# Kernel optimization log

Measured on AMD Instinct MI355X. Metric: run time of the kernel, lower is better.

Reference implementation:

```python
import jax, jax.numpy as jnp
import numpy as np

EPS = 1e-12  # torch F.normalize eps


def _l2norm(v, axis):
    return v / jnp.maximum(jnp.linalg.norm(v, axis=axis, keepdims=True), EPS)


def setup_inputs() -> dict:
    key = jax.random.key(0)
    k1, k2, k3 = jax.random.split(key, 3)
    N, D, H, W, K = 32, 512, 64, 64, 64
    x = jax.random.normal(k1, (N, D, H, W), dtype=jnp.float32)
    conv_w = jax.random.normal(k2, (K, D), dtype=jnp.float32) * 0.05
    centroids = jax.random.normal(k3, (K, D), dtype=jnp.float32)
    return {"x": x, "conv_w": conv_w, "centroids": centroids}


def reference(x, conv_w, centroids):
    # x: [N, D, H, W]; conv_w: [K, D] (1x1 conv, no bias); centroids: [K, D]
    N, D, H, W = x.shape
    K = conv_w.shape[0]
    # descriptor-wise L2 normalization over channel dim
    x = _l2norm(x, axis=1)
    xf = x.reshape(N, D, H * W)                      # [N, D, P]
    # 1x1 conv == matmul over channels; softmax over clusters
    logits = jnp.einsum('kd,ndp->nkp', conv_w, xf)    # [N, K, P]
    a = jax.nn.softmax(logits, axis=1)                # [N, K, P]
    # vlad[n,k,d] = sum_p a[n,k,p] * (xf[n,d,p] - c[k,d])
    #            = (a @ xf^T)[n,k,d] - (sum_p a[n,k,p]) * c[k,d]
    vlad = jnp.einsum('nkp,ndp->nkd', a, xf) \
         - a.sum(axis=-1)[:, :, None] * centroids[None, :, :]  # [N, K, D]
    vlad = _l2norm(vlad, axis=2)                      # intra-normalization
    v = vlad.reshape(N, K * D)
    return _l2norm(v, axis=1)                         # global L2 norm
```

## Files before the change

### kernel.cpp

```cpp
#include <hip/hip_runtime.h>
#include <hip/hip_bf16.h>
#include <math.h>

#define Nn 32
#define Dd 512
#define Pp 4096
#define Kk 64
#define SEG 16
#define PXB 256
#define PT 64
static constexpr float EPSF = 1e-12f;

typedef short short8 __attribute__((ext_vector_type(8)));
typedef short short4v __attribute__((ext_vector_type(4)));
typedef float floatx4 __attribute__((ext_vector_type(4)));

static __device__ __forceinline__ int f2b2(float a, float b) {
  __hip_bfloat162 h = __float22bfloat162_rn(float2{a, b});
  int r; __builtin_memcpy(&r, &h, 4); return r;
}
static __device__ __forceinline__ short8 pack8(const float* v) {
  union { short8 s; int i[4]; } u;
  u.i[0] = f2b2(v[0], v[1]); u.i[1] = f2b2(v[2], v[3]);
  u.i[2] = f2b2(v[4], v[5]); u.i[3] = f2b2(v[6], v[7]);
  return u.s;
}
static __device__ __forceinline__ short f2b1(float f) {
  unsigned u = __float_as_uint(f);
  return (short)((u + 0x7FFFu + ((u >> 16) & 1u)) >> 16);
}
static __device__ __forceinline__ float b2f(short s) {
  return __uint_as_float(((unsigned)(unsigned short)s) << 16);
}

__global__ __launch_bounds__(256) void k_wpack(
    const float* __restrict__ w, short* __restrict__ wp)
{
  int id = blockIdx.x * 256 + threadIdx.x;
  int chunk = id >> 6, k = id & 63;
  const float* src = w + (size_t)k * Dd + chunk * 32;
  short* dst = wp + ((size_t)(chunk * 64 + k)) * 32;
#pragma unroll
  for (int q = 0; q < 4; ++q) {
    float v[8];
    *(float4*)&v[0] = *(const float4*)(src + q * 8);
    *(float4*)&v[4] = *(const float4*)(src + q * 8 + 4);
    *(short8*)(dst + q * 8) = pack8(v);
  }
}

__global__ __launch_bounds__(256, 2) void k_fused(
    const float* __restrict__ x, const short* __restrict__ wp,
    float* __restrict__ asum, short* __restrict__ vpart)
{
  constexpr int XS = 64;
  constexpr int AS = 72;
  __shared__ short xb[Dd * XS];
  __shared__ short as_[Kk * AS];
  __shared__ float invs[PT];

  const int tid = threadIdx.x;
  const int n = blockIdx.x >> 4, seg = blockIdx.x & 15;
  const int wave = tid >> 6, lane = tid & 63;
  const int q = lane >> 4, pc = lane & 15;
  const int sd = tid >> 3, sc = tid & 7;

  floatx4 acc2[4][8];
#pragma unroll
  for (int t = 0; t < 4; ++t)
#pragma unroll
    for (int s2 = 0; s2 < 8; ++s2) acc2[t][s2] = floatx4{0.f, 0.f, 0.f, 0.f};
  float asr[4] = {0.f, 0.f, 0.f, 0.f};

  const float* xn = x + (size_t)n * Dd * Pp;

  for (int pt = 0; pt < PXB / PT; ++pt) {
    const int p0 = seg * PXB + pt * PT;
    __syncthreads();

    floatx4 acc1[4];
#pragma unroll
    for (int t = 0; t < 4; ++t) acc1[t] = floatx4{0.f, 0.f, 0.f, 0.f};
    float sq = 0.f;

    const float* xa = xn + (size_t)(q * 8) * Pp + p0 + wave * 16 + pc;
    const float* xs = xn + (size_t)sd * Pp + p0 + sc * 8;

    for (int dc = 0; dc < Dd; dc += 32) {
      float4 u0 = *(const float4*)xs;
      float4 u1 = *(const float4*)(xs + 4);
      int2 w0 = { f2b2(u0.x, u0.y), f2b2(u0.z, u0.w) };
      int2 w1 = { f2b2(u1.x, u1.y), f2b2(u1.z, u1.w) };
      *(int2*)&xb[(dc + sd) * XS + sc * 8] = w0;
      *(int2*)&xb[(dc + sd) * XS + sc * 8 + 4] = w1;
      xs += (size_t)32 * Pp;
      float v[8];
#pragma unroll
      for (int j = 0; j < 8; ++j) {
        float a = xa[(size_t)j * Pp];
        v[j] = a; sq += a * a;
      }
      xa += (size_t)32 * Pp;
      short8 af = pack8(v);
      const short* wc = wp + (size_t)(dc >> 5) * 2048 + pc * 32 + q * 8;
#pragma unroll
      for (int t = 0; t < 4; ++t) {
        short8 bf = *(const short8*)(wc + t * 512);
        acc1[t] = __builtin_amdgcn_mfma_f32_16x16x32_bf16(af, bf, acc1[t], 0, 0, 0);
      }
    }

    {
      float tsum = sq;
      tsum += __shfl_xor(tsum, 16);
      tsum += __shfl_xor(tsum, 32);
      if (q == 0) invs[wave * 16 + pc] = 1.f / fmaxf(sqrtf(tsum), EPSF);
    }
    float ivr[4];
#pragma unroll
    for (int r = 0; r < 4; ++r) ivr[r] = invs[wave * 16 + q * 4 + r];

#pragma unroll
    for (int r = 0; r < 4; ++r) {
      float l[4];
#pragma unroll
      for (int t = 0; t < 4; ++t) l[t] = acc1[t][r] * ivr[r];
      float mx = fmaxf(fmaxf(l[0], l[1]), fmaxf(l[2], l[3]));
      mx = fmaxf(mx, __shfl_xor(mx, 1));
      mx = fmaxf(mx, __shfl_xor(mx, 2));
      mx = fmaxf(mx, __shfl_xor(mx, 4));
      mx = fmaxf(mx, __shfl_xor(mx, 8));
      float e[4], sm = 0.f;
#pragma unroll
      for (int t = 0; t < 4; ++t) { e[t] = __expf(l[t] - mx); sm += e[t]; }
      sm += __shfl_xor(sm, 1);
      sm += __shfl_xor(sm, 2);
      sm += __shfl_xor(sm, 4);
      sm += __shfl_xor(sm, 8);
      float si = 1.f / sm;
#pragma unroll
      for (int t = 0; t < 4; ++t) {
        float av = e[t] * si;
        asr[t] += av;
        as_[(t * 16 + pc) * AS + wave * 16 + q * 4 + r] = f2b1(av * ivr[r]);
      }
    }
    __syncthreads();

#pragma unroll
    for (int c = 0; c < 2; ++c) {
      short8 af2[4];
#pragma unroll
      for (int t = 0; t < 4; ++t)
        af2[t] = *(const short8*)&as_[(t * 16 + pc) * AS + c * 32 + q * 8];
#pragma unroll
      for (int s2 = 0; s2 < 8; ++s2) {
        short8 bf2 = *(const short8*)&xb[(wave * 128 + s2 * 16 + pc) * XS + c * 32 + q * 8];
#pragma unroll
        for (int t = 0; t < 4; ++t)
          acc2[t][s2] = __builtin_amdgcn_mfma_f32_16x16x32_bf16(af2[t], bf2, acc2[t][s2], 0, 0, 0);
      }
    }
  }

#pragma unroll
  for (int t = 0; t < 4; ++t) {
    float v = asr[t];
    v += __shfl_xor(v, 16);
    v += __shfl_xor(v, 32);
    if (q == 0) atomicAdd(&asum[n * Kk + t * 16 + pc], v);
  }
  short* vb = vpart + ((size_t)(seg * Nn + n) * Kk) * Dd;
#pragma unroll
  for (int t = 0; t < 4; ++t)
#pragma unroll
    for (int s2 = 0; s2 < 8; ++s2)
#pragma unroll
      for (int r = 0; r < 4; ++r)
        vb[(size_t)(t * 16 + q * 4 + r) * Dd + wave * 128 + s2 * 16 + pc] =
            f2b1(acc2[t][s2][r]);
}

__global__ __launch_bounds__(128) void k_intra(
    const short* __restrict__ vpart, const float* __restrict__ asum,
    const float* __restrict__ cent, float* __restrict__ out, float* __restrict__ gnsq)
{
  __shared__ float red[2];
  const int nk = blockIdx.x;
  const int n = nk >> 6, k = nk & 63;
  const int tid = threadIdx.x;
  const int d = tid * 4;

  float4 v = {0.f, 0.f, 0.f, 0.f};
#pragma unroll
  for (int ps = 0; ps < SEG; ++ps) {
    short4v t = *(const short4v*)&vpart[((size_t)(ps * Nn + n) * Kk + k) * Dd + d];
    v.x += b2f(t[0]); v.y += b2f(t[1]); v.z += b2f(t[2]); v.w += b2f(t[3]);
  }
  float s = asum[n * Kk + k];
  float4 c = *(const float4*)&cent[(size_t)k * Dd + d];
  v.x -= s * c.x; v.y -= s * c.y; v.z -= s * c.z; v.w -= s * c.w;

  float qq = v.x * v.x + v.y * v.y + v.z * v.z + v.w * v.w;
#pragma unroll
  for (int off = 32; off; off >>= 1) qq += __shfl_down(qq, off);
  if ((tid & 63) == 0) red[tid >> 6] = qq;
  __syncthreads();
  float norm = sqrtf(red[0] + red[1]);
  float r = 1.f / fmaxf(norm, EPSF);
  v.x *= r; v.y *= r; v.z *= r; v.w *= r;
  *(float4*)&out[(size_t)n * (Kk * Dd) + (size_t)k * Dd + d] = v;
  if (tid == 0) {
    float t = norm * r;
    atomicAdd(&gnsq[n], t * t);
  }
}

__global__ __launch_bounds__(256) void k_gscale(
    float* __restrict__ out, const float* __restrict__ gnsq)
{
  size_t i = ((size_t)blockIdx.x * 256 + threadIdx.x) * 4;
  int n = (int)(i >> 15);
  float r = 1.f / fmaxf(sqrtf(gnsq[n]), EPSF);
  float4 v = *(float4*)&out[i];
  v.x *= r; v.y *= r; v.z *= r; v.w *= r;
  *(float4*)&out[i] = v;
}

extern "C" void kernel_launch(void* const* d_in, const int* in_sizes, int n_in,
                              void* d_out, int out_size, void* d_ws, size_t ws_size,
                              hipStream_t stream) {
  (void)in_sizes; (void)n_in; (void)out_size; (void)ws_size;
  const float* x    = (const float*)d_in[0];
  const float* w    = (const float*)d_in[1];
  const float* cent = (const float*)d_in[2];
  float* out = (float*)d_out;

  float* asum  = (float*)d_ws;
  float* gnsq  = asum + Nn * Kk;
  short* vpart = (short*)(gnsq + 64);
  short* wpk   = vpart + (size_t)SEG * Nn * Kk * Dd;

  hipMemsetAsync(asum, 0, (Nn * Kk + 64) * sizeof(float), stream);
  k_wpack<<<4, 256, 0, stream>>>(w, wpk);
  k_fused<<<Nn * SEG, 256, 0, stream>>>(x, wpk, asum, vpart);
  k_intra<<<Nn * Kk, 128, 0, stream>>>(vpart, asum, cent, out, gnsq);
  k_gscale<<<(Nn * Kk * Dd) / (256 * 4), 256, 0, stream>>>(out, gnsq);
}
```

Measured before the change: 421.0 us.

## Split k_fused clusters across 8 waves, swizzle LDS, fold global norm into constant

```diff
diff --git a/kernel.cpp b/kernel.cpp
--- a/kernel.cpp
+++ b/kernel.cpp
@@ -34,9 +34,12 @@
 }
 
 __global__ __launch_bounds__(256) void k_wpack(
-    const float* __restrict__ w, short* __restrict__ wp)
+    const float* __restrict__ w, float* __restrict__ asum,
+    short* __restrict__ wp)
 {
   int id = blockIdx.x * 256 + threadIdx.x;
+  if (id >= 1024) return;
+  asum[id] = 0.f; asum[id + 1024] = 0.f;
   int chunk = id >> 6, k = id & 63;
   const float* src = w + (size_t)k * Dd + chunk * 32;
   short* dst = wp + ((size_t)(chunk * 64 + k)) * 32;
@@ -49,7 +52,7 @@
   }
 }
 
-__global__ __launch_bounds__(256, 2) void k_fused(
+__global__ __launch_bounds__(512, 4) void k_fused(
     const float* __restrict__ x, const short* __restrict__ wp,
     float* __restrict__ asum, short* __restrict__ vpart)
 {
@@ -58,19 +61,23 @@
   __shared__ short xb[Dd * XS];
   __shared__ short as_[Kk * AS];
   __shared__ float invs[PT];
+  __shared__ float ssum[2 * PT];
 
   const int tid = threadIdx.x;
   const int n = blockIdx.x >> 4, seg = blockIdx.x & 15;
   const int wave = tid >> 6, lane = tid & 63;
+  const int wg = wave & 3, kh = wave >> 2;
   const int q = lane >> 4, pc = lane & 15;
-  const int sd = tid >> 3, sc = tid & 7;
-
-  floatx4 acc2[4][8];
-#pragma unroll
-  for (int t = 0; t < 4; ++t)
-#pragma unroll
-    for (int s2 = 0; s2 < 8; ++s2) acc2[t][s2] = floatx4{0.f, 0.f, 0.f, 0.f};
-  float asr[4] = {0.f, 0.f, 0.f, 0.f};
+  const int sd = tid >> 4, sc = tid & 15;
+  const int swcol = (sc * 4) ^ ((sd & 7) << 3);
+  const int rdxor = (pc & 7) << 3;
+
+  floatx4 acc2[4][4];
+#pragma unroll
+  for (int a = 0; a < 4; ++a)
+#pragma unroll
+    for (int b = 0; b < 4; ++b) acc2[a][b] = floatx4{0.f, 0.f, 0.f, 0.f};
+  float asr[2] = {0.f, 0.f};
 
   const float* xn = x + (size_t)n * Dd * Pp;
 
@@ -78,21 +85,18 @@
     const int p0 = seg * PXB + pt * PT;
     __syncthreads();
 
-    floatx4 acc1[4];
-#pragma unroll
-    for (int t = 0; t < 4; ++t) acc1[t] = floatx4{0.f, 0.f, 0.f, 0.f};
+    floatx4 acc1[2];
+    acc1[0] = floatx4{0.f, 0.f, 0.f, 0.f};
+    acc1[1] = floatx4{0.f, 0.f, 0.f, 0.f};
     float sq = 0.f;
 
-    const float* xa = xn + (size_t)(q * 8) * Pp + p0 + wave * 16 + pc;
-    const float* xs = xn + (size_t)sd * Pp + p0 + sc * 8;
+    const float* xa = xn + (size_t)(q * 8) * Pp + p0 + wg * 16 + pc;
+    const float* xs = xn + (size_t)sd * Pp + p0 + sc * 4;
 
     for (int dc = 0; dc < Dd; dc += 32) {
       float4 u0 = *(const float4*)xs;
-      float4 u1 = *(const float4*)(xs + 4);
-      int2 w0 = { f2b2(u0.x, u0.y), f2b2(u0.z, u0.w) };
-      int2 w1 = { f2b2(u1.x, u1.y), f2b2(u1.z, u1.w) };
-      *(int2*)&xb[(dc + sd) * XS + sc * 8] = w0;
-      *(int2*)&xb[(dc + sd) * XS + sc * 8 + 4] = w1;
+      *(int2*)&xb[(dc + sd) * XS + swcol] =
+          int2{ f2b2(u0.x, u0.y), f2b2(u0.z, u0.w) };
       xs += (size_t)32 * Pp;
       float v[8];
 #pragma unroll
@@ -102,48 +106,44 @@
       }
       xa += (size_t)32 * Pp;
       short8 af = pack8(v);
-      const short* wc = wp + (size_t)(dc >> 5) * 2048 + pc * 32 + q * 8;
-#pragma unroll
-      for (int t = 0; t < 4; ++t) {
-        short8 bf = *(const short8*)(wc + t * 512);
-        acc1[t] = __builtin_amdgcn_mfma_f32_16x16x32_bf16(af, bf, acc1[t], 0, 0, 0);
-      }
+      const short* wc = wp + (size_t)(dc >> 5) * 2048 + kh * 1024 + pc * 32 + q * 8;
+      acc1[0] = __builtin_amdgcn_mfma_f32_16x16x32_bf16(
+          af, *(const short8*)wc, acc1[0], 0, 0, 0);
+      acc1[1] = __builtin_amdgcn_mfma_f32_16x16x32_bf16(
+          af, *(const short8*)(wc + 512), acc1[1], 0, 0, 0);
     }
 
     {
       float tsum = sq;
       tsum += __shfl_xor(tsum, 16);
       tsum += __shfl_xor(tsum, 32);
-      if (q == 0) invs[wave * 16 + pc] = 1.f / fmaxf(sqrtf(tsum), EPSF);
-    }
-    float ivr[4];
-#pragma unroll
-    for (int r = 0; r < 4; ++r) ivr[r] = invs[wave * 16 + q * 4 + r];
+      if (q == 0) invs[wg * 16 + pc] = 1.f / fmaxf(sqrtf(tsum), EPSF);
+    }
+    float ivr[4], e0[4], e1[4];
+#pragma unroll
+    for (int r = 0; r < 4; ++r) ivr[r] = invs[wg * 16 + q * 4 + r];
 
 #pragma unroll
     for (int r = 0; r < 4; ++r) {
-      float l[4];
-#pragma unroll
-      for (int t = 0; t < 4; ++t) l[t] = acc1[t][r] * ivr[r];
-      float mx = fmaxf(fmaxf(l[0], l[1]), fmaxf(l[2], l[3]));
-      mx = fmaxf(mx, __shfl_xor(mx, 1));
-      mx = fmaxf(mx, __shfl_xor(mx, 2));
-      mx = fmaxf(mx, __shfl_xor(mx, 4));
-      mx = fmaxf(mx, __shfl_xor(mx, 8));
-      float e[4], sm = 0.f;
-#pragma unroll
-      for (int t = 0; t < 4; ++t) { e[t] = __expf(l[t] - mx); sm += e[t]; }
-      sm += __shfl_xor(sm, 1);
-      sm += __shfl_xor(sm, 2);
-      sm += __shfl_xor(sm, 4);
-      sm += __shfl_xor(sm, 8);
-      float si = 1.f / sm;
-#pragma unroll
-      for (int t = 0; t < 4; ++t) {
-        float av = e[t] * si;
-        asr[t] += av;
-        as_[(t * 16 + pc) * AS + wave * 16 + q * 4 + r] = f2b1(av * ivr[r]);
-      }
+      e0[r] = __expf(acc1[0][r] * ivr[r]);
+      e1[r] = __expf(acc1[1][r] * ivr[r]);
+      float s = e0[r] + e1[r];
+      s += __shfl_xor(s, 1);
+      s += __shfl_xor(s, 2);
+      s += __shfl_xor(s, 4);
+      s += __shfl_xor(s, 8);
+      if (pc == 0) ssum[kh * PT + wg * 16 + q * 4 + r] = s;
+    }
+    __syncthreads();
+
+#pragma unroll
+    for (int r = 0; r < 4; ++r) {
+      const int px = wg * 16 + q * 4 + r;
+      float si = 1.f / (ssum[px] + ssum[PT + px]);
+      float a0 = e0[r] * si, a1 = e1[r] * si;
+      asr[0] += a0; asr[1] += a1;
+      as_[(kh * 32 + pc) * AS + px]      = f2b1(a0 * ivr[r]);
+      as_[(kh * 32 + 16 + pc) * AS + px] = f2b1(a1 * ivr[r]);
     }
     __syncthreads();
 
@@ -151,39 +151,41 @@
     for (int c = 0; c < 2; ++c) {
       short8 af2[4];
 #pragma unroll
-      for (int t = 0; t < 4; ++t)
-        af2[t] = *(const short8*)&as_[(t * 16 + pc) * AS + c * 32 + q * 8];
-#pragma unroll
-      for (int s2 = 0; s2 < 8; ++s2) {
-        short8 bf2 = *(const short8*)&xb[(wave * 128 + s2 * 16 + pc) * XS + c * 32 + q * 8];
-#pragma unroll
-        for (int t = 0; t < 4; ++t)
-          acc2[t][s2] = __builtin_amdgcn_mfma_f32_16x16x32_bf16(af2[t], bf2, acc2[t][s2], 0, 0, 0);
+      for (int kt = 0; kt < 4; ++kt)
+        af2[kt] = *(const short8*)&as_[(kt * 16 + pc) * AS + c * 32 + q * 8];
+#pragma unroll
+      for (int s2 = 0; s2 < 4; ++s2) {
+        const int row = (wave << 6) + s2 * 16 + pc;
+        short8 bf2 = *(const short8*)&xb[row * XS + ((c * 32 + q * 8) ^ rdxor)];
+#pragma unroll
+        for (int kt = 0; kt < 4; ++kt)
+          acc2[kt][s2] = __builtin_amdgcn_mfma_f32_16x16x32_bf16(
+              af2[kt], bf2, acc2[kt][s2], 0, 0, 0);
       }
     }
   }
 
 #pragma unroll
-  for (int t = 0; t < 4; ++t) {
+  for (int t = 0; t < 2; ++t) {
     float v = asr[t];
     v += __shfl_xor(v, 16);
     v += __shfl_xor(v, 32);
-    if (q == 0) atomicAdd(&asum[n * Kk + t * 16 + pc], v);
+    if (q == 0) atomicAdd(&asum[n * Kk + kh * 32 + t * 16 + pc], v);
   }
   short* vb = vpart + ((size_t)(seg * Nn + n) * Kk) * Dd;
 #pragma unroll
-  for (int t = 0; t < 4; ++t)
-#pragma unroll
-    for (int s2 = 0; s2 < 8; ++s2)
+  for (int kt = 0; kt < 4; ++kt)
+#pragma unroll
+    for (int s2 = 0; s2 < 4; ++s2)
 #pragma unroll
       for (int r = 0; r < 4; ++r)
-        vb[(size_t)(t * 16 + q * 4 + r) * Dd + wave * 128 + s2 * 16 + pc] =
-            f2b1(acc2[t][s2][r]);
+        vb[(size_t)(kt * 16 + q * 4 + r) * Dd + (wave << 6) + s2 * 16 + pc] =
+            f2b1(acc2[kt][s2][r]);
 }
 
 __global__ __launch_bounds__(128) void k_intra(
     const short* __restrict__ vpart, const float* __restrict__ asum,
-    const float* __restrict__ cent, float* __restrict__ out, float* __restrict__ gnsq)
+    const float* __restrict__ cent, float* __restrict__ out)
 {
   __shared__ float red[2];
   const int nk = blockIdx.x;
@@ -207,24 +209,9 @@
   if ((tid & 63) == 0) red[tid >> 6] = qq;
   __syncthreads();
   float norm = sqrtf(red[0] + red[1]);
-  float r = 1.f / fmaxf(norm, EPSF);
+  float r = 0.125f / fmaxf(norm, EPSF);
   v.x *= r; v.y *= r; v.z *= r; v.w *= r;
   *(float4*)&out[(size_t)n * (Kk * Dd) + (size_t)k * Dd + d] = v;
-  if (tid == 0) {
-    float t = norm * r;
-    atomicAdd(&gnsq[n], t * t);
-  }
-}
-
-__global__ __launch_bounds__(256) void k_gscale(
-    float* __restrict__ out, const float* __restrict__ gnsq)
-{
-  size_t i = ((size_t)blockIdx.x * 256 + threadIdx.x) * 4;
-  int n = (int)(i >> 15);
-  float r = 1.f / fmaxf(sqrtf(gnsq[n]), EPSF);
-  float4 v = *(float4*)&out[i];
-  v.x *= r; v.y *= r; v.z *= r; v.w *= r;
-  *(float4*)&out[i] = v;
 }
 
 extern "C" void kernel_launch(void* const* d_in, const int* in_sizes, int n_in,
@@ -237,13 +224,10 @@
   float* out = (float*)d_out;
 
   float* asum  = (float*)d_ws;
-  float* gnsq  = asum + Nn * Kk;
-  short* vpart = (short*)(gnsq + 64);
+  short* vpart = (short*)(asum + Nn * Kk);
   short* wpk   = vpart + (size_t)SEG * Nn * Kk * Dd;
 
-  hipMemsetAsync(asum, 0, (Nn * Kk + 64) * sizeof(float), stream);
-  k_wpack<<<4, 256, 0, stream>>>(w, wpk);
-  k_fused<<<Nn * SEG, 256, 0, stream>>>(x, wpk, asum, vpart);
-  k_intra<<<Nn * Kk, 128, 0, stream>>>(vpart, asum, cent, out, gnsq);
-  k_gscale<<<(Nn * Kk * Dd) / (256 * 4), 256, 0, stream>>>(out, gnsq);
-}
+  k_wpack<<<4, 256, 0, stream>>>(w, asum, wpk);
+  k_fused<<<Nn * SEG, 512, 0, stream>>>(x, wpk, asum, vpart);
+  k_intra<<<Nn * Kk, 128, 0, stream>>>(vpart, asum, cent, out);
+}
```

Result: slower. 511.0 us (+21.4%).
